# Performance work log

Measured on AMD Instinct MI355X. Metric: run time of the kernel, lower is better.

Reference implementation:

```python
import jax, jax.numpy as jnp
import numpy as np

N_LAYERS = 3
NUM_USERS = 100_000
NUM_ITEMS = 100_000
EMB_DIM = 64
NNZ = 2_000_000


def setup_inputs() -> dict:
    key = jax.random.key(0)
    k1, k2, k3, k4, k5 = jax.random.split(key, 5)
    n_nodes = NUM_USERS + 1 + NUM_ITEMS  # 200001
    user_emb = jax.random.normal(k1, (NUM_USERS + 1, EMB_DIM), dtype=jnp.float32) * 0.1
    user_emb = user_emb.at[0].set(0.0)  # padding_idx=0
    item_emb = jax.random.normal(k2, (NUM_ITEMS + 1, EMB_DIM), dtype=jnp.float32) * 0.1
    item_emb = item_emb.at[0].set(0.0)  # padding_idx=0
    adj_rows = jax.random.randint(k3, (NNZ,), 0, n_nodes, dtype=jnp.int32)
    adj_cols = jax.random.randint(k4, (NNZ,), 0, n_nodes, dtype=jnp.int32)
    # symmetric-normalized adjacency values are small positive numbers
    adj_vals = jax.random.uniform(k5, (NNZ,), dtype=jnp.float32) * 0.1
    return {
        "user_emb": user_emb,
        "item_emb": item_emb,
        "adj_rows": adj_rows,
        "adj_cols": adj_cols,
        "adj_vals": adj_vals,
    }


def _spmm(adj_rows, adj_cols, adj_vals, x, n_nodes):
    # y[r] = sum over nnz with row==r of val * x[col]  (COO SpMM)
    msgs = adj_vals[:, None] * x[adj_cols]  # [nnz, d]
    return jax.ops.segment_sum(msgs, adj_rows, num_segments=n_nodes)


def reference(user_emb, item_emb, adj_rows, adj_cols, adj_vals):
    n_users_p1 = user_emb.shape[0]
    all_emb = jnp.concatenate([user_emb, item_emb[1:]], axis=0)  # [N, d]
    n_nodes = all_emb.shape[0]
    acc = all_emb  # running sum for layer-mean pooling
    x = all_emb
    for _ in range(N_LAYERS):
        x = _spmm(adj_rows, adj_cols, adj_vals, x, n_nodes)
        acc = acc + x
    all_out = acc / jnp.asarray(N_LAYERS + 1, all_emb.dtype)
    user_out = all_out[:n_users_p1]
    item_out = jnp.concatenate(
        [jnp.zeros((1, all_out.shape[1]), all_out.dtype), all_out[n_users_p1:]], axis=0
    )
    return user_out, item_out
```

## Files before the change

### kernel.cpp

```cpp
#include <hip/hip_runtime.h>


#define N_NODES 200001
#define NUP1    100001
#define D       64
#define DV      16
#define DV8     8
#define CHUNK   512
#define NCHUNK  ((N_NODES + CHUNK - 1) / CHUNK)
#define T_TILE  4096
#define EPT     16
#define CAP     6144
#define REP     2
#define HALFCAP (CAP / REP)
#define CNT_STRIDE 16
#define CNT_TOTAL  (NCHUNK * REP * CNT_STRIDE)

__device__ __forceinline__ unsigned short f2bf(float f) {
  unsigned u = __float_as_uint(f);
  unsigned r = (u + 0x7FFFu + ((u >> 16) & 1u)) >> 16;
  return (unsigned short)r;
}
__device__ __forceinline__ float bf2f(unsigned short h) {
  return __uint_as_float(((unsigned)h) << 16);
}
__device__ __forceinline__ float bflo(unsigned u) { return __uint_as_float(u << 16); }
__device__ __forceinline__ float bfhi(unsigned u) { return __uint_as_float(u & 0xFFFF0000u); }

__global__ __launch_bounds__(256) void init_kernel(
    const float4* __restrict__ user_emb,
    const float4* __restrict__ item_emb,
    ushort4* __restrict__ x0,
    int* __restrict__ bucket_cnt) {
  int idx = blockIdx.x * 256 + threadIdx.x;
  if (idx < CNT_TOTAL) bucket_cnt[idx] = 0;
  if (idx >= N_NODES * DV) return;
  int n = idx >> 4;
  int j = idx & 15;
  float4 v = (n < NUP1) ? user_emb[idx]
                        : item_emb[(size_t)(n - 100000) * DV + j];
  x0[idx] = make_ushort4(f2bf(v.x), f2bf(v.y), f2bf(v.z), f2bf(v.w));
}

__global__ __launch_bounds__(256) void pass1_bucket(
    const int*   __restrict__ rows,
    const int*   __restrict__ cols,
    const float* __restrict__ vals,
    int*  __restrict__ bucket_cnt,
    int2* __restrict__ bucket_arr,
    int nnz) {
  __shared__ int lcount[NCHUNK];
  __shared__ int lbase[NCHUNK];
  int t = threadIdx.x;
  for (int i = t; i < NCHUNK; i += 256) lcount[i] = 0;
  __syncthreads();
  long base = (long)blockIdx.x * T_TILE;
  int rep = blockIdx.x & (REP - 1);
  int2 pk[EPT];
  int  meta[EPT];
#pragma unroll
  for (int k = 0; k < EPT; ++k) {
    long e = base + t + (long)k * 256;
    if (e < nnz) {
      int r = rows[e];
      int b = r >> 9;
      int rank = atomicAdd(&lcount[b], 1);
      pk[k] = make_int2(((r & 511) << 18) | cols[e], __float_as_int(vals[e]));
      meta[k] = (rank << 9) | b;
    } else {
      meta[k] = -1;
    }
  }
  __syncthreads();
  for (int b = t; b < NCHUNK; b += 256) {
    int c = lcount[b];
    lbase[b] = (c > 0)
        ? (b * CAP + rep * HALFCAP +
           atomicAdd(&bucket_cnt[(b * REP + rep) * CNT_STRIDE], c))
        : 0;
  }
  __syncthreads();
#pragma unroll
  for (int k = 0; k < EPT; ++k) {
    if (meta[k] >= 0) {
      int b = meta[k] & 511;
      int rank = meta[k] >> 9;
      bucket_arr[lbase[b] + rank] = pk[k];
    }
  }
}

__global__ __launch_bounds__(512) void scan_chunks_kernel(
    const int* __restrict__ cnt, int* __restrict__ off,
    int* __restrict__ row_ptr, int nnz) {
  __shared__ int sh[512];
  int t = threadIdx.x;
  int v = (t < NCHUNK)
      ? cnt[(t * REP + 0) * CNT_STRIDE] + cnt[(t * REP + 1) * CNT_STRIDE]
      : 0;
  sh[t] = v;
  __syncthreads();
  for (int o = 1; o < 512; o <<= 1) {
    int u = (t >= o) ? sh[t - o] : 0;
    __syncthreads();
    sh[t] += u;
    __syncthreads();
  }
  if (t < NCHUNK) off[t] = sh[t] - v;
  if (t == 0) row_ptr[N_NODES] = nnz;
}

__global__ __launch_bounds__(256) void build_csr_chunk(
    const int*  __restrict__ bucket_cnt,
    const int2* __restrict__ bucket_arr,
    const int*  __restrict__ chunk_off,
    int*  __restrict__ row_ptr,
    int2* __restrict__ edge_s) {
  __shared__ int lcnt[CHUNK];
  __shared__ int tsum[256];
  int b = blockIdx.x, t = threadIdx.x;
  lcnt[t] = 0; lcnt[t + 256] = 0;
  __syncthreads();
  int ne0 = bucket_cnt[(b * REP + 0) * CNT_STRIDE];
  int ne1 = bucket_cnt[(b * REP + 1) * CNT_STRIDE];
  const int2* ba = bucket_arr + (size_t)b * CAP;
  for (int i = t; i < ne0; i += 256)
    atomicAdd(&lcnt[ba[i].x >> 18], 1);
  for (int i = t; i < ne1; i += 256)
    atomicAdd(&lcnt[ba[HALFCAP + i].x >> 18], 1);
  __syncthreads();
  int base = t * 2;
  int l0 = lcnt[base], l1 = lcnt[base + 1];
  int s = l0 + l1;
  tsum[t] = s;
  __syncthreads();
  for (int o = 1; o < 256; o <<= 1) {
    int v = (t >= o) ? tsum[t - o] : 0;
    __syncthreads();
    tsum[t] += v;
    __syncthreads();
  }
  int run = tsum[t] - s + chunk_off[b];
  int row0 = b * CHUNK;
  if (row0 + base < N_NODES) row_ptr[row0 + base] = run;
  lcnt[base] = run;
  run += l0;
  if (row0 + base + 1 < N_NODES) row_ptr[row0 + base + 1] = run;
  lcnt[base + 1] = run;
  __syncthreads();
  for (int i = t; i < ne0; i += 256) {
    int2 ed = ba[i];
    int p = atomicAdd(&lcnt[ed.x >> 18], 1);
    edge_s[p] = make_int2(ed.x & 0x3FFFF, ed.y);
  }
  for (int i = t; i < ne1; i += 256) {
    int2 ed = ba[HALFCAP + i];
    int p = atomicAdd(&lcnt[ed.x >> 18], 1);
    edge_s[p] = make_int2(ed.x & 0x3FFFF, ed.y);
  }
}

#define SPMM_BODY                                                   \
  int t = blockIdx.x * 256 + threadIdx.x;                           \
  int r = t >> 3;                                                   \
  int j = t & 7;                                                    \
  float a0 = 0.f, a1 = 0.f, a2 = 0.f, a3 = 0.f;                     \
  float a4 = 0.f, a5 = 0.f, a6 = 0.f, a7 = 0.f;                     \
  {                                                                 \
    int s = row_ptr[r];                                             \
    int e = row_ptr[r + 1];                                         \
    int last = e - 1;                                               \
    for (int g = s; g < e; g += 8) {                                \
      int2 e0 = edge_s[min(g + 0, last)];                           \
      int2 e1 = edge_s[min(g + 1, last)];                           \
      int2 e2 = edge_s[min(g + 2, last)];                           \
      int2 e3 = edge_s[min(g + 3, last)];                           \
      int2 e4 = edge_s[min(g + 4, last)];                           \
      int2 e5 = edge_s[min(g + 5, last)];                           \
      int2 e6 = edge_s[min(g + 6, last)];                           \
      int2 e7 = edge_s[min(g + 7, last)];                           \
      uint4 x0 = x[(size_t)e0.x * DV8 + j];                         \
      uint4 x1 = x[(size_t)e1.x * DV8 + j];                         \
      uint4 x2 = x[(size_t)e2.x * DV8 + j];                         \
      uint4 x3 = x[(size_t)e3.x * DV8 + j];                         \
      uint4 x4 = x[(size_t)e4.x * DV8 + j];                         \
      uint4 x5 = x[(size_t)e5.x * DV8 + j];                         \
      uint4 x6 = x[(size_t)e6.x * DV8 + j];                         \
      uint4 x7 = x[(size_t)e7.x * DV8 + j];                         \
      float v0 = __int_as_float(e0.y);                              \
      float v1 = (g + 1 < e) ? __int_as_float(e1.y) : 0.f;          \
      float v2 = (g + 2 < e) ? __int_as_float(e2.y) : 0.f;          \
      float v3 = (g + 3 < e) ? __int_as_float(e3.y) : 0.f;          \
      float v4 = (g + 4 < e) ? __int_as_float(e4.y) : 0.f;          \
      float v5 = (g + 5 < e) ? __int_as_float(e5.y) : 0.f;          \
      float v6 = (g + 6 < e) ? __int_as_float(e6.y) : 0.f;          \
      float v7 = (g + 7 < e) ? __int_as_float(e7.y) : 0.f;          \
      ACCUM(v0, x0); ACCUM(v1, x1); ACCUM(v2, x2); ACCUM(v3, x3);   \
      ACCUM(v4, x4); ACCUM(v5, x5); ACCUM(v6, x6); ACCUM(v7, x7);   \
    }                                                               \
  }

#define ACCUM(V, XV) {                                    \
    a0 += (V) * bflo((XV).x); a1 += (V) * bfhi((XV).x);   \
    a2 += (V) * bflo((XV).y); a3 += (V) * bfhi((XV).y);   \
    a4 += (V) * bflo((XV).z); a5 += (V) * bfhi((XV).z);   \
    a6 += (V) * bflo((XV).w); a7 += (V) * bfhi((XV).w); }

__global__ __launch_bounds__(256) void spmm_bf16_kernel(
    const int*  __restrict__ row_ptr,
    const int2* __restrict__ edge_s,
    const uint4* __restrict__ x,
    uint4*       __restrict__ y) {
  if ((blockIdx.x * 256 + threadIdx.x) >> 3 >= N_NODES) return;
  SPMM_BODY
  uint4 o;
  o.x = ((unsigned)f2bf(a1) << 16) | f2bf(a0);
  o.y = ((unsigned)f2bf(a3) << 16) | f2bf(a2);
  o.z = ((unsigned)f2bf(a5) << 16) | f2bf(a4);
  o.w = ((unsigned)f2bf(a7) << 16) | f2bf(a6);
  y[t] = o;
}

__global__ __launch_bounds__(256) void spmm_final_kernel(
    const int*  __restrict__ row_ptr,
    const int2* __restrict__ edge_s,
    const uint4* __restrict__ x,
    const uint4* __restrict__ y1u,
    const float4* __restrict__ user_emb,
    const float4* __restrict__ item_emb,
    float4* __restrict__ out) {
  int gt = blockIdx.x * 256 + threadIdx.x;
  if (gt < DV) out[(size_t)NUP1 * DV + gt] = make_float4(0.f, 0.f, 0.f, 0.f);
  if (gt >> 3 >= N_NODES) return;
  SPMM_BODY
  uint4 w1 = y1u[(size_t)r * DV8 + j];
  uint4 w2 = x  [(size_t)r * DV8 + j];
  int rm = (r < NUP1) ? r : r + 1;
  size_t eb = (size_t)r * DV + 2 * j;
  float4 f0, f1;
  if (r < NUP1) {
    f0 = user_emb[eb];
    f1 = user_emb[eb + 1];
  } else {
    size_t ib = (size_t)(r - 100000) * DV + 2 * j;
    f0 = item_emb[ib];
    f1 = item_emb[ib + 1];
  }
  float4 o0, o1;
  o0.x = 0.25f * (f0.x + bflo(w1.x) + bflo(w2.x) + a0);
  o0.y = 0.25f * (f0.y + bfhi(w1.x) + bfhi(w2.x) + a1);
  o0.z = 0.25f * (f0.z + bflo(w1.y) + bflo(w2.y) + a2);
  o0.w = 0.25f * (f0.w + bfhi(w1.y) + bfhi(w2.y) + a3);
  o1.x = 0.25f * (f1.x + bflo(w1.z) + bflo(w2.z) + a4);
  o1.y = 0.25f * (f1.y + bfhi(w1.z) + bfhi(w2.z) + a5);
  o1.z = 0.25f * (f1.z + bflo(w1.w) + bflo(w2.w) + a6);
  o1.w = 0.25f * (f1.w + bfhi(w1.w) + bfhi(w2.w) + a7);
  out[(size_t)rm * DV + 2 * j]     = o0;
  out[(size_t)rm * DV + 2 * j + 1] = o1;
}
#undef ACCUM

static inline char* align16(char* p) {
  return (char*)(((uintptr_t)p + 15) & ~(uintptr_t)15);
}

extern "C" void kernel_launch(void* const* d_in, const int* in_sizes, int n_in,
                              void* d_out, int out_size, void* d_ws, size_t ws_size,
                              hipStream_t stream) {
  const float* user_emb = (const float*)d_in[0];
  const float* item_emb = (const float*)d_in[1];
  const int*   rows     = (const int*)d_in[2];
  const int*   cols     = (const int*)d_in[3];
  const float* vals     = (const float*)d_in[4];
  const int    nnz      = in_sizes[2];

  const size_t xbytes = (size_t)N_NODES * D * sizeof(unsigned short);
  char* p = (char*)d_ws;
  ushort4* x0 = (ushort4*)p;  p += xbytes;
  ushort4* y1 = (ushort4*)p;  p += xbytes;
  ushort4* y2 = (ushort4*)p;  p += xbytes;
  ushort4* y3 = (ushort4*)p;  p += xbytes;
  int2* bucket_arr = (int2*)y2;
  (void)y3;
  p = align16(p);
  int2* edge_s = (int2*)p;    p += (size_t)nnz * sizeof(int2);
  p = align16(p);
  int* row_ptr = (int*)p;     p += (size_t)(N_NODES + 1) * sizeof(int);
  p = align16(p);
  int* chunk_off = (int*)p;   p += (size_t)NCHUNK * sizeof(int);
  p = align16(p);
  int* bucket_cnt = (int*)p;  p += (size_t)CNT_TOTAL * sizeof(int);

  float* out = (float*)d_out;

  const int row_elems = N_NODES * DV;
  const int node_grid = (row_elems + 255) / 256;
  const int spmm_grid = (N_NODES * DV8 + 255) / 256;
  const int tile_grid = (nnz + T_TILE - 1) / T_TILE;

  init_kernel<<<node_grid, 256, 0, stream>>>(
      (const float4*)user_emb, (const float4*)item_emb, x0, bucket_cnt);
  pass1_bucket<<<tile_grid, 256, 0, stream>>>(
      rows, cols, vals, bucket_cnt, bucket_arr, nnz);
  scan_chunks_kernel<<<1, 512, 0, stream>>>(bucket_cnt, chunk_off, row_ptr, nnz);
  build_csr_chunk<<<NCHUNK, 256, 0, stream>>>(
      bucket_cnt, bucket_arr, chunk_off, row_ptr, edge_s);

  spmm_bf16_kernel<<<spmm_grid, 256, 0, stream>>>(
      row_ptr, edge_s, (const uint4*)x0, (uint4*)y1);
  spmm_bf16_kernel<<<spmm_grid, 256, 0, stream>>>(
      row_ptr, edge_s, (const uint4*)y1, (uint4*)y2);
  spmm_final_kernel<<<spmm_grid, 256, 0, stream>>>(
      row_ptr, edge_s, (const uint4*)y2, (const uint4*)y1,
      (const float4*)user_emb, (const float4*)item_emb, (float4*)out);
}
```

Before: 312.8 us.

## Merge init and bucketing kernels and fold chunk scan into CSR build

Combines the embedding bf16 conversion and the edge bucketing pass into one launch with a block-index split, and replaces the counter-zeroing in init with a memset. The single-block chunk-offset scan kernel is removed; every build_csr_chunk block now recomputes the full prefix over all chunk counts in shared memory. This removes two kernel launches and their serialization gaps, at the cost of a redundant scan per block and an extra memset operation.

```diff
diff --git a/kernel.cpp b/kernel.cpp
--- a/kernel.cpp
+++ b/kernel.cpp
@@ -27,31 +27,29 @@
 __device__ __forceinline__ float bflo(unsigned u) { return __uint_as_float(u << 16); }
 __device__ __forceinline__ float bfhi(unsigned u) { return __uint_as_float(u & 0xFFFF0000u); }
 
-__global__ __launch_bounds__(256) void init_kernel(
+__global__ __launch_bounds__(256) void setup_kernel(
     const float4* __restrict__ user_emb,
     const float4* __restrict__ item_emb,
     ushort4* __restrict__ x0,
-    int* __restrict__ bucket_cnt) {
-  int idx = blockIdx.x * 256 + threadIdx.x;
-  if (idx < CNT_TOTAL) bucket_cnt[idx] = 0;
-  if (idx >= N_NODES * DV) return;
-  int n = idx >> 4;
-  int j = idx & 15;
-  float4 v = (n < NUP1) ? user_emb[idx]
-                        : item_emb[(size_t)(n - 100000) * DV + j];
-  x0[idx] = make_ushort4(f2bf(v.x), f2bf(v.y), f2bf(v.z), f2bf(v.w));
-}
-
-__global__ __launch_bounds__(256) void pass1_bucket(
     const int*   __restrict__ rows,
     const int*   __restrict__ cols,
     const float* __restrict__ vals,
     int*  __restrict__ bucket_cnt,
     int2* __restrict__ bucket_arr,
-    int nnz) {
+    int nnz, int tile_grid) {
   __shared__ int lcount[NCHUNK];
   __shared__ int lbase[NCHUNK];
   int t = threadIdx.x;
+  if (blockIdx.x >= tile_grid) {
+    int idx = (blockIdx.x - tile_grid) * 256 + t;
+    if (idx >= N_NODES * DV) return;
+    int n = idx >> 4;
+    int j = idx & 15;
+    float4 v = (n < NUP1) ? user_emb[idx]
+                          : item_emb[(size_t)(n - 100000) * DV + j];
+    x0[idx] = make_ushort4(f2bf(v.x), f2bf(v.y), f2bf(v.z), f2bf(v.w));
+    return;
+  }
   for (int i = t; i < NCHUNK; i += 256) lcount[i] = 0;
   __syncthreads();
   long base = (long)blockIdx.x * T_TILE;
@@ -90,35 +88,38 @@
   }
 }
 
-__global__ __launch_bounds__(512) void scan_chunks_kernel(
-    const int* __restrict__ cnt, int* __restrict__ off,
-    int* __restrict__ row_ptr, int nnz) {
-  __shared__ int sh[512];
-  int t = threadIdx.x;
-  int v = (t < NCHUNK)
-      ? cnt[(t * REP + 0) * CNT_STRIDE] + cnt[(t * REP + 1) * CNT_STRIDE]
-      : 0;
-  sh[t] = v;
-  __syncthreads();
-  for (int o = 1; o < 512; o <<= 1) {
-    int u = (t >= o) ? sh[t - o] : 0;
-    __syncthreads();
-    sh[t] += u;
-    __syncthreads();
-  }
-  if (t < NCHUNK) off[t] = sh[t] - v;
-  if (t == 0) row_ptr[N_NODES] = nnz;
-}
-
 __global__ __launch_bounds__(256) void build_csr_chunk(
     const int*  __restrict__ bucket_cnt,
     const int2* __restrict__ bucket_arr,
-    const int*  __restrict__ chunk_off,
     int*  __restrict__ row_ptr,
-    int2* __restrict__ edge_s) {
+    int2* __restrict__ edge_s, int nnz) {
   __shared__ int lcnt[CHUNK];
   __shared__ int tsum[256];
+  __shared__ int sc0[256];
+  __shared__ int poff[256];
   int b = blockIdx.x, t = threadIdx.x;
+  int i0 = 2 * t, i1 = 2 * t + 1;
+  int c0 = (i0 < NCHUNK)
+      ? bucket_cnt[(i0 * REP + 0) * CNT_STRIDE] +
+        bucket_cnt[(i0 * REP + 1) * CNT_STRIDE] : 0;
+  int c1 = (i1 < NCHUNK)
+      ? bucket_cnt[(i1 * REP + 0) * CNT_STRIDE] +
+        bucket_cnt[(i1 * REP + 1) * CNT_STRIDE] : 0;
+  int ps = c0 + c1;
+  sc0[t] = c0;
+  tsum[t] = ps;
+  __syncthreads();
+  for (int o = 1; o < 256; o <<= 1) {
+    int v = (t >= o) ? tsum[t - o] : 0;
+    __syncthreads();
+    tsum[t] += v;
+    __syncthreads();
+  }
+  poff[t] = tsum[t] - ps;
+  __syncthreads();
+  int chunk_off_b = poff[b >> 1] + ((b & 1) ? sc0[b >> 1] : 0);
+  if (b == 0 && t == 0) row_ptr[N_NODES] = nnz;
+  __syncthreads();
   lcnt[t] = 0; lcnt[t + 256] = 0;
   __syncthreads();
   int ne0 = bucket_cnt[(b * REP + 0) * CNT_STRIDE];
@@ -140,7 +141,7 @@
     tsum[t] += v;
     __syncthreads();
   }
-  int run = tsum[t] - s + chunk_off[b];
+  int run = tsum[t] - s + chunk_off_b;
   int row0 = b * CHUNK;
   if (row0 + base < N_NODES) row_ptr[row0 + base] = run;
   lcnt[base] = run;
@@ -287,8 +288,6 @@
   p = align16(p);
   int* row_ptr = (int*)p;     p += (size_t)(N_NODES + 1) * sizeof(int);
   p = align16(p);
-  int* chunk_off = (int*)p;   p += (size_t)NCHUNK * sizeof(int);
-  p = align16(p);
   int* bucket_cnt = (int*)p;  p += (size_t)CNT_TOTAL * sizeof(int);
 
   float* out = (float*)d_out;
@@ -298,13 +297,12 @@
   const int spmm_grid = (N_NODES * DV8 + 255) / 256;
   const int tile_grid = (nnz + T_TILE - 1) / T_TILE;
 
-  init_kernel<<<node_grid, 256, 0, stream>>>(
-      (const float4*)user_emb, (const float4*)item_emb, x0, bucket_cnt);
-  pass1_bucket<<<tile_grid, 256, 0, stream>>>(
-      rows, cols, vals, bucket_cnt, bucket_arr, nnz);
-  scan_chunks_kernel<<<1, 512, 0, stream>>>(bucket_cnt, chunk_off, row_ptr, nnz);
+  hipMemsetAsync(bucket_cnt, 0, (size_t)CNT_TOTAL * sizeof(int), stream);
+  setup_kernel<<<tile_grid + node_grid, 256, 0, stream>>>(
+      (const float4*)user_emb, (const float4*)item_emb, x0,
+      rows, cols, vals, bucket_cnt, bucket_arr, nnz, tile_grid);
   build_csr_chunk<<<NCHUNK, 256, 0, stream>>>(
-      bucket_cnt, bucket_arr, chunk_off, row_ptr, edge_s);
+      bucket_cnt, bucket_arr, row_ptr, edge_s, nnz);
 
   spmm_bf16_kernel<<<spmm_grid, 256, 0, stream>>>(
       row_ptr, edge_s, (const uint4*)x0, (uint4*)y1);
```

After: 305.5 us. -2.3%, faster.
